# Kernel optimization log

Hardware: AMD Instinct MI355X
Metric: run time of the kernel (lower is better)

Reference implementation:

```python
import jax, jax.numpy as jnp
import numpy as np

D_MODEL = 1024
N_HEADS_Q = 16
N_HEADS_KV = 4
D_HEAD = 64  # d_qk = d_v
THETA = 10000.0
CLAMP = 80.0


def apply_rope(x, theta=THETA):
    # x: (b, h, s, d) with d even; interleaved-pair rotary embedding
    b, h, s, d = x.shape
    inv_freq = 1.0 / (theta ** (jnp.arange(0, d, 2, dtype=jnp.float32) / d))  # (d/2,)
    ang = jnp.arange(s, dtype=jnp.float32)[:, None] * inv_freq[None, :]       # (s, d/2)
    cos, sin = jnp.cos(ang), jnp.sin(ang)
    x1, x2 = x[..., 0::2], x[..., 1::2]
    o1 = x1 * cos - x2 * sin
    o2 = x1 * sin + x2 * cos
    return jnp.stack([o1, o2], axis=-1).reshape(b, h, s, d).astype(x.dtype)


def setup_inputs() -> dict:
    key = jax.random.key(0)
    k0, k1, k2, k3, k4 = jax.random.split(key, 5)
    scale = 1.0 / np.sqrt(D_MODEL)
    return {
        "x": jax.random.normal(k0, (2, 2048, D_MODEL), dtype=jnp.float32),
        "Wq": jax.random.normal(k1, (N_HEADS_Q * D_HEAD, D_MODEL), dtype=jnp.float32) * scale,
        "Wk": jax.random.normal(k2, (N_HEADS_KV * D_HEAD, D_MODEL), dtype=jnp.float32) * scale,
        "Wv": jax.random.normal(k3, (N_HEADS_KV * D_HEAD, D_MODEL), dtype=jnp.float32) * scale,
        "Wo": jax.random.normal(k4, (D_MODEL, N_HEADS_Q * D_HEAD), dtype=jnp.float32) * scale,
    }


def _attention(x, Wq, Wk, Wv, Wo):
    b, s, _ = x.shape
    r = N_HEADS_Q // N_HEADS_KV  # queries per KV group
    # projections (Linear: y = x @ W^T, no bias)
    Q = (x @ Wq.T).reshape(b, s, N_HEADS_Q, D_HEAD).transpose(0, 2, 1, 3)   # (b, Hq, s, d)
    K = (x @ Wk.T).reshape(b, s, N_HEADS_KV, D_HEAD).transpose(0, 2, 1, 3)  # (b, Hkv, s, d)
    V = (x @ Wv.T).reshape(b, s, N_HEADS_KV, D_HEAD).transpose(0, 2, 1, 3)
    Q = apply_rope(Q)
    K = apply_rope(K)
    # GQA grouping: (b, Hkv, r, s, d)
    Qg = Q.reshape(b, N_HEADS_KV, r, s, D_HEAD)
    scores = jnp.einsum('bgrqd,bgkd->bgrqk', Qg, K)          # (b, g, r, s, s)
    scores = jnp.clip(scores, -CLAMP, CLAMP)
    causal = jnp.tril(jnp.ones((s, s), dtype=bool))
    scores = jnp.where(causal, scores, -jnp.inf)
    weights = jax.nn.softmax(scores / jnp.sqrt(jnp.float32(D_HEAD)), axis=-1)
    attn = jnp.einsum('bgrqk,bgkd->bgrqd', weights, V)       # (b, g, r, s, d)
    # '... h_kv r s d -> ... s (h_kv r d)'
    attn = attn.transpose(0, 3, 1, 2, 4).reshape(b, s, N_HEADS_Q * D_HEAD)
    return attn @ Wo.T


def reference(x, Wq, Wk, Wv, Wo):
    return _attention(x, Wq, Wk, Wv, Wo)
```

## Files before the change

### kernel.cpp

```cpp
#include <hip/hip_runtime.h>
#include <hip/hip_bf16.h>
#include <math.h>

typedef __attribute__((ext_vector_type(8))) short bf16x8;
typedef __attribute__((ext_vector_type(4))) float f32x4;

#define B_   2
#define S_   2048
#define DM   1024
#define HQ   16
#define HKV  4
#define DH   64

#define MFMA16(a, b, c) __builtin_amdgcn_mfma_f32_16x16x32_bf16(a, b, c, 0, 0, 0)

__device__ __forceinline__ void load_lds16(const __hip_bfloat16* g, __hip_bfloat16* l)
{
    __builtin_amdgcn_global_load_lds(
        (const __attribute__((address_space(1))) unsigned int*)g,
        (__attribute__((address_space(3))) unsigned int*)l, 16, 0, 0);
}

#define CVT_TOTAL 6815744
__global__ void cvt_all(const float* __restrict__ x,  const float* __restrict__ wq,
                        const float* __restrict__ wk, const float* __restrict__ wv,
                        const float* __restrict__ wo,
                        __hip_bfloat16* __restrict__ xb,  __hip_bfloat16* __restrict__ wqb,
                        __hip_bfloat16* __restrict__ wkb, __hip_bfloat16* __restrict__ wvb,
                        __hip_bfloat16* __restrict__ wob)
{
    int i = (blockIdx.x * blockDim.x + threadIdx.x) * 4;
    if (i >= CVT_TOTAL) return;
    const float* src; __hip_bfloat16* dst; int off;
    if      (i < 4194304) { src = x;  dst = xb;  off = 0; }
    else if (i < 5242880) { src = wq; dst = wqb; off = 4194304; }
    else if (i < 5505024) { src = wk; dst = wkb; off = 5242880; }
    else if (i < 5767168) { src = wv; dst = wvb; off = 5505024; }
    else                  { src = wo; dst = wob; off = 5767168; }
    i -= off;
    float4 v = *(const float4*)(src + i);
    union { ushort4 u; __hip_bfloat16 h[4]; } p;
    p.h[0] = __float2bfloat16(v.x);
    p.h[1] = __float2bfloat16(v.y);
    p.h[2] = __float2bfloat16(v.z);
    p.h[3] = __float2bfloat16(v.w);
    *(ushort4*)(dst + i) = p.u;
}

template <bool QKV>
__global__ __launch_bounds__(256, 3) void gemm_tile(
    const __hip_bfloat16* __restrict__ A,
    const __hip_bfloat16* __restrict__ W,
    float* __restrict__ C0, __hip_bfloat16* __restrict__ Qb,
    __hip_bfloat16* __restrict__ Kb, __hip_bfloat16* __restrict__ Vt, int K)
{
    const int wave = threadIdx.x >> 6;
    const int lane = threadIdx.x & 63;
    const int quad = lane >> 4;
    const int l16  = lane & 15;
    const int wm = wave >> 1, wn = wave & 1;
    const int m0 = blockIdx.x * 64;
    const int n0 = blockIdx.y * 128;

    __shared__ __align__(16) __hip_bfloat16 As[64 * 32];
    __shared__ __align__(16) __hip_bfloat16 Bs[128 * 32];

    f32x4 acc[2][4] = {};

    for (int k0 = 0; k0 < K; k0 += 32) {
        #pragma unroll
        for (int r = 0; r < 3; ++r) {
            const int m = wave * 3 + r;
            if (m < 4) {
                const int g = m * 64 + lane;
                const int row = g >> 2;
                const int cbs = ((g & 3) - row) & 3;
                load_lds16(A + (size_t)(m0 + row) * K + k0 + cbs * 8, &As[m * 512]);
            } else {
                const int g = (m - 4) * 64 + lane;
                const int row = g >> 2;
                const int cbs = ((g & 3) - row) & 3;
                load_lds16(W + (size_t)(n0 + row) * K + k0 + cbs * 8, &Bs[(m - 4) * 512]);
            }
        }
        __syncthreads();
        bf16x8 af[2], bf[4];
        #pragma unroll
        for (int i = 0; i < 2; ++i) {
            const int ra = wm * 32 + i * 16 + l16;
            af[i] = *(const bf16x8*)&As[ra * 32 + ((quad + ra) & 3) * 8];
        }
        #pragma unroll
        for (int j = 0; j < 4; ++j) {
            const int rb = wn * 64 + j * 16 + l16;
            bf[j] = *(const bf16x8*)&Bs[rb * 32 + ((quad + rb) & 3) * 8];
        }
        #pragma unroll
        for (int i = 0; i < 2; ++i)
            #pragma unroll
            for (int j = 0; j < 4; ++j)
                acc[i][j] = MFMA16(af[i], bf[j], acc[i][j]);
        __syncthreads();
    }

    #pragma unroll
    for (int j = 0; j < 4; ++j) {
        const int cbase = n0 + wn * 64 + j * 16;
        const int cb = cbase + l16;
        if (QKV && cbase < 1280) {
            const int ii = (cb >> 1) & 31;
            const float f = exp2f((float)ii * -0.41524101186092f);
            const float f_rev = f * 0.15915494309189535f;
            const bool odd = cb & 1;
            #pragma unroll
            for (int i = 0; i < 2; ++i) {
                #pragma unroll
                for (int reg = 0; reg < 4; ++reg) {
                    const int row = m0 + wm * 32 + i * 16 + quad * 4 + reg;
                    const float v = acc[i][j][reg];
                    const float p = __shfl_xor(v, 1);
                    float rev = (float)(row & (S_ - 1)) * f_rev;
                    rev -= floorf(rev);
                    const float sn = __builtin_amdgcn_sinf(rev);
                    const float cs = __builtin_amdgcn_cosf(rev);
                    const float o = odd ? (p * sn + v * cs) : (v * cs - p * sn);
                    if (cbase < 1024)
                        Qb[(size_t)row * 1024 + cb] = __float2bfloat16(o);
                    else
                        Kb[(size_t)row * 256 + cb - 1024] = __float2bfloat16(o);
                }
            }
        } else {
            #pragma unroll
            for (int i = 0; i < 2; ++i) {
                #pragma unroll
                for (int reg = 0; reg < 4; ++reg) {
                    const int row = m0 + wm * 32 + i * 16 + quad * 4 + reg;
                    const float v = acc[i][j][reg];
                    if (QKV)
                        Vt[((size_t)(row >> 11) * 256 + (cb - 1280)) * S_ +
                           (row & (S_ - 1))] = __float2bfloat16(v);
                    else
                        C0[(size_t)row * 1024 + cb] = v;
                }
            }
        }
    }
}

template <bool MASKED>
__device__ __forceinline__ void softmax_store(
    const f32x4* sacc, int q, int k0, int quad, int l16,
    float& lsum, __hip_bfloat16* PsTile)
{
    #pragma unroll
    for (int nt = 0; nt < 4; ++nt) {
        union { ushort4 u; __hip_bfloat16 h[4]; } pk;
        #pragma unroll
        for (int reg = 0; reg < 4; ++reg) {
            const float sc = fminf(fmaxf(sacc[nt][reg], -80.0f), 80.0f);
            float p = exp2f(fmaf(sc, 0.18033688011112042f,
                                 -14.426950408889634f));
            if (MASKED) {
                const int key = k0 + nt * 16 + quad * 4 + reg;
                p = (key <= q) ? p : 0.0f;
            }
            lsum += p;
            pk.h[reg] = __float2bfloat16(p);
        }
        *(ushort4*)&PsTile[l16 * 72 + nt * 16 + quad * 4] = pk.u;
    }
}

__global__ __launch_bounds__(256, 2) void attn_mfma(
    const __hip_bfloat16* __restrict__ Q,
    const __hip_bfloat16* __restrict__ K,
    const __hip_bfloat16* __restrict__ Vt,
    __hip_bfloat16* __restrict__ ctx)
{
    const int t    = blockIdx.x & 15;
    const int hq   = (blockIdx.x >> 4) & (HQ - 1);
    const int b    = blockIdx.x >> 8;
    const int hkv  = hq >> 2;
    const int wave = threadIdx.x >> 6;
    const int lane = threadIdx.x & 63;
    const int quad = lane >> 4;
    const int l16  = lane & 15;

    const int qlo = t * 64 + wave * 16 + l16;
    const int qhi = (31 - t) * 64 + wave * 16 + l16;

    __shared__ __align__(16) __hip_bfloat16 Ks[2][64 * 64];
    __shared__ __align__(16) __hip_bfloat16 Vs[2][64 * 64];
    __shared__ __align__(16) __hip_bfloat16 Ps[4][2][16 * 72];

    const __hip_bfloat16* qpl = Q + ((size_t)(b * S_) + qlo) * (HQ * DH) + hq * DH + quad * 8;
    const __hip_bfloat16* qph = Q + ((size_t)(b * S_) + qhi) * (HQ * DH) + hq * DH + quad * 8;
    bf16x8 ql0 = *(const bf16x8*)qpl;
    bf16x8 ql1 = *(const bf16x8*)(qpl + 32);
    bf16x8 qh0 = *(const bf16x8*)qph;
    bf16x8 qh1 = *(const bf16x8*)(qph + 32);

    const __hip_bfloat16* Kg = K + (size_t)(b * S_) * (HKV * DH) + hkv * DH;
    const __hip_bfloat16* Vg = Vt + (size_t)(b * HKV + hkv) * DH * S_;

    auto stage = [&](int sb, int k0s) {
        #pragma unroll
        for (int r = 0; r < 2; ++r) {
            const int m = wave * 2 + r;
            const int g = m * 64 + lane;
            const int row = g >> 3;
            const int cbs = ((g & 7) - row) & 7;
            load_lds16(Kg + (size_t)(k0s + row) * (HKV * DH) + cbs * 8, &Ks[sb][m * 512]);
            load_lds16(Vg + (size_t)row * S_ + k0s + cbs * 8, &Vs[sb][m * 512]);
        }
    };

    stage(0, 0);

    float lsum_lo = 0.0f, lsum_hi = 0.0f;
    f32x4 Olo[4] = {}, Ohi[4] = {};
    const f32x4 zro = {0.0f, 0.0f, 0.0f, 0.0f};

    const int last = 31 - t;
    for (int kt = 0; kt <= last; ++kt) {
        const int buf = kt & 1;
        const int k0 = kt * 64;
        __syncthreads();
        if (kt < last) stage(buf ^ 1, k0 + 64);
        const bool dual = (kt <= t);

        bf16x8 ka[4][2];
        #pragma unroll
        for (int nt = 0; nt < 4; ++nt) {
            const int key = nt * 16 + l16;
            ka[nt][0] = *(const bf16x8*)&Ks[buf][key * 64 + ((quad + key) & 7) * 8];
            ka[nt][1] = *(const bf16x8*)&Ks[buf][key * 64 + ((quad + 4 + key) & 7) * 8];
        }
        f32x4 shi[4], slo[4];
        #pragma unroll
        for (int nt = 0; nt < 4; ++nt) {
            shi[nt] = MFMA16(ka[nt][0], qh0, zro);
            shi[nt] = MFMA16(ka[nt][1], qh1, shi[nt]);
        }
        if (dual) {
            #pragma unroll
            for (int nt = 0; nt < 4; ++nt) {
                slo[nt] = MFMA16(ka[nt][0], ql0, zro);
                slo[nt] = MFMA16(ka[nt][1], ql1, slo[nt]);
            }
        }

        if (kt == last) softmax_store<true >(shi, qhi, k0, quad, l16, lsum_hi, &Ps[wave][1][0]);
        else            softmax_store<false>(shi, qhi, k0, quad, l16, lsum_hi, &Ps[wave][1][0]);
        if (dual) {
            if (kt == t) softmax_store<true >(slo, qlo, k0, quad, l16, lsum_lo, &Ps[wave][0][0]);
            else         softmax_store<false>(slo, qlo, k0, quad, l16, lsum_lo, &Ps[wave][0][0]);
        }
        __asm__ __volatile__("s_waitcnt lgkmcnt(0)" ::: "memory");

        bf16x8 va[2][4];
        #pragma unroll
        for (int ks = 0; ks < 2; ++ks)
            #pragma unroll
            for (int dt = 0; dt < 4; ++dt) {
                const int d = dt * 16 + l16;
                va[ks][dt] = *(const bf16x8*)
                    &Vs[buf][d * 64 + ((ks * 4 + quad + d) & 7) * 8];
            }
        #pragma unroll
        for (int ks = 0; ks < 2; ++ks) {
            bf16x8 pb = *(const bf16x8*)&Ps[wave][1][l16 * 72 + ks * 32 + quad * 8];
            #pragma unroll
            for (int dt = 0; dt < 4; ++dt)
                Ohi[dt] = MFMA16(va[ks][dt], pb, Ohi[dt]);
        }
        if (dual) {
            #pragma unroll
            for (int ks = 0; ks < 2; ++ks) {
                bf16x8 pb = *(const bf16x8*)&Ps[wave][0][l16 * 72 + ks * 32 + quad * 8];
                #pragma unroll
                for (int dt = 0; dt < 4; ++dt)
                    Olo[dt] = MFMA16(va[ks][dt], pb, Olo[dt]);
            }
        }
    }

    auto finish = [&](float lsum, const f32x4* O, int qrow) {
        lsum += __shfl_xor(lsum, 16);
        lsum += __shfl_xor(lsum, 32);
        const float inv = 1.0f / lsum;
        __hip_bfloat16* cp =
            ctx + ((size_t)(b * S_) + qrow) * (HQ * DH) + hq * DH + quad * 4;
        #pragma unroll
        for (int dt = 0; dt < 4; ++dt) {
            union { ushort4 u; __hip_bfloat16 h[4]; } o;
            #pragma unroll
            for (int reg = 0; reg < 4; ++reg)
                o.h[reg] = __float2bfloat16(O[dt][reg] * inv);
            *(ushort4*)(cp + dt * 16) = o.u;
        }
    };
    finish(lsum_lo, Olo, qlo);
    finish(lsum_hi, Ohi, qhi);
}

extern "C" void kernel_launch(void* const* d_in, const int* in_sizes, int n_in,
                              void* d_out, int out_size, void* d_ws, size_t ws_size,
                              hipStream_t stream)
{
    const float* x  = (const float*)d_in[0];
    const float* Wq = (const float*)d_in[1];
    const float* Wk = (const float*)d_in[2];
    const float* Wv = (const float*)d_in[3];
    const float* Wo = (const float*)d_in[4];
    float* out = (float*)d_out;

    const int M = B_ * S_;

    char* w = (char*)d_ws;
    __hip_bfloat16* xb    = (__hip_bfloat16*)w;  w += (size_t)M * DM * 2;
    __hip_bfloat16* Wqkvb = (__hip_bfloat16*)w;  w += (size_t)1536 * DM * 2;
    __hip_bfloat16* Wob   = (__hip_bfloat16*)w;  w += (size_t)DM * (HQ * DH) * 2;
    __hip_bfloat16* Qb16  = (__hip_bfloat16*)w;  w += (size_t)M * (HQ * DH) * 2;
    __hip_bfloat16* Kb16  = (__hip_bfloat16*)w;  w += (size_t)M * (HKV * DH) * 2;
    __hip_bfloat16* Vt    = (__hip_bfloat16*)w;  w += (size_t)M * (HKV * DH) * 2;
    __hip_bfloat16* ctx   = (__hip_bfloat16*)w;

    __hip_bfloat16* Wqb = Wqkvb;
    __hip_bfloat16* Wkb = Wqkvb + (size_t)1024 * 1024;
    __hip_bfloat16* Wvb = Wqkvb + (size_t)1280 * 1024;

    cvt_all<<<(CVT_TOTAL / 4 + 255) / 256, 256, 0, stream>>>(
        x, Wq, Wk, Wv, Wo, xb, Wqb, Wkb, Wvb, Wob);

    gemm_tile<true><<<dim3(M / 64, 1536 / 128), 256, 0, stream>>>(
        xb, Wqkvb, nullptr, Qb16, Kb16, Vt, DM);

    attn_mfma<<<B_ * HQ * 16, 256, 0, stream>>>(Qb16, Kb16, Vt, ctx);

    gemm_tile<false><<<dim3(M / 64, 1024 / 128), 256, 0, stream>>>(
        ctx, Wob, out, nullptr, nullptr, nullptr, HQ * DH);
}
```

Before: 173.4 us.

## Load V fragments directly from global memory and swap PV MFMA operand order

V tiles are no longer staged through LDS. Each lane now loads its V^T fragments straight from global memory into registers at the start of each key tile, and the PV MFMA operands are swapped so P is the A operand. The output layout therefore changes: the finish step shuffles the per-row normalizer and writes scalar bf16 elements instead of ushort4 vectors. This removes the LDS traffic and footprint for V, which could help occupancy, but it adds uncached-latency global loads per iteration and less coalesced scalar stores.

```diff
diff --git a/kernel.cpp b/kernel.cpp
--- a/kernel.cpp
+++ b/kernel.cpp
@@ -187,11 +187,12 @@
     const int quad = lane >> 4;
     const int l16  = lane & 15;
 
-    const int qlo = t * 64 + wave * 16 + l16;
-    const int qhi = (31 - t) * 64 + wave * 16 + l16;
+    const int qb_lo = t * 64 + wave * 16;
+    const int qb_hi = (31 - t) * 64 + wave * 16;
+    const int qlo = qb_lo + l16;
+    const int qhi = qb_hi + l16;
 
     __shared__ __align__(16) __hip_bfloat16 Ks[2][64 * 64];
-    __shared__ __align__(16) __hip_bfloat16 Vs[2][64 * 64];
     __shared__ __align__(16) __hip_bfloat16 Ps[4][2][16 * 72];
 
     const __hip_bfloat16* qpl = Q + ((size_t)(b * S_) + qlo) * (HQ * DH) + hq * DH + quad * 8;
@@ -202,7 +203,8 @@
     bf16x8 qh1 = *(const bf16x8*)(qph + 32);
 
     const __hip_bfloat16* Kg = K + (size_t)(b * S_) * (HKV * DH) + hkv * DH;
-    const __hip_bfloat16* Vg = Vt + (size_t)(b * HKV + hkv) * DH * S_;
+    const __hip_bfloat16* Vb =
+        Vt + ((size_t)(b * HKV + hkv) * DH + l16) * S_ + quad * 8;
 
     auto stage = [&](int sb, int k0s) {
         #pragma unroll
@@ -212,7 +214,6 @@
             const int row = g >> 3;
             const int cbs = ((g & 7) - row) & 7;
             load_lds16(Kg + (size_t)(k0s + row) * (HKV * DH) + cbs * 8, &Ks[sb][m * 512]);
-            load_lds16(Vg + (size_t)row * S_ + k0s + cbs * 8, &Vs[sb][m * 512]);
         }
     };
 
@@ -230,6 +231,13 @@
         if (kt < last) stage(buf ^ 1, k0 + 64);
         const bool dual = (kt <= t);
 
+        bf16x8 vb[2][4];
+        #pragma unroll
+        for (int ks = 0; ks < 2; ++ks)
+            #pragma unroll
+            for (int dt = 0; dt < 4; ++dt)
+                vb[ks][dt] = *(const bf16x8*)(Vb + (size_t)dt * 16 * S_ + k0 + ks * 32);
+
         bf16x8 ka[4][2];
         #pragma unroll
         for (int nt = 0; nt < 4; ++nt) {
@@ -259,50 +267,40 @@
         }
         __asm__ __volatile__("s_waitcnt lgkmcnt(0)" ::: "memory");
 
-        bf16x8 va[2][4];
-        #pragma unroll
-        for (int ks = 0; ks < 2; ++ks)
-            #pragma unroll
-            for (int dt = 0; dt < 4; ++dt) {
-                const int d = dt * 16 + l16;
-                va[ks][dt] = *(const bf16x8*)
-                    &Vs[buf][d * 64 + ((ks * 4 + quad + d) & 7) * 8];
-            }
         #pragma unroll
         for (int ks = 0; ks < 2; ++ks) {
-            bf16x8 pb = *(const bf16x8*)&Ps[wave][1][l16 * 72 + ks * 32 + quad * 8];
+            bf16x8 pa = *(const bf16x8*)&Ps[wave][1][l16 * 72 + ks * 32 + quad * 8];
             #pragma unroll
             for (int dt = 0; dt < 4; ++dt)
-                Ohi[dt] = MFMA16(va[ks][dt], pb, Ohi[dt]);
+                Ohi[dt] = MFMA16(pa, vb[ks][dt], Ohi[dt]);
         }
         if (dual) {
             #pragma unroll
             for (int ks = 0; ks < 2; ++ks) {
-                bf16x8 pb = *(const bf16x8*)&Ps[wave][0][l16 * 72 + ks * 32 + quad * 8];
+                bf16x8 pa = *(const bf16x8*)&Ps[wave][0][l16 * 72 + ks * 32 + quad * 8];
                 #pragma unroll
                 for (int dt = 0; dt < 4; ++dt)
-                    Olo[dt] = MFMA16(va[ks][dt], pb, Olo[dt]);
+                    Olo[dt] = MFMA16(pa, vb[ks][dt], Olo[dt]);
             }
         }
     }
 
-    auto finish = [&](float lsum, const f32x4* O, int qrow) {
+    auto finish = [&](float lsum, const f32x4* O, int qbase) {
         lsum += __shfl_xor(lsum, 16);
         lsum += __shfl_xor(lsum, 32);
         const float inv = 1.0f / lsum;
-        __hip_bfloat16* cp =
-            ctx + ((size_t)(b * S_) + qrow) * (HQ * DH) + hq * DH + quad * 4;
-        #pragma unroll
-        for (int dt = 0; dt < 4; ++dt) {
-            union { ushort4 u; __hip_bfloat16 h[4]; } o;
-            #pragma unroll
-            for (int reg = 0; reg < 4; ++reg)
-                o.h[reg] = __float2bfloat16(O[dt][reg] * inv);
-            *(ushort4*)(cp + dt * 16) = o.u;
+        #pragma unroll
+        for (int reg = 0; reg < 4; ++reg) {
+            const float invr = __shfl(inv, quad * 4 + reg);
+            const int q = qbase + quad * 4 + reg;
+            __hip_bfloat16* cp = ctx + ((size_t)(b * S_) + q) * (HQ * DH) + hq * DH + l16;
+            #pragma unroll
+            for (int dt = 0; dt < 4; ++dt)
+                cp[dt * 16] = __float2bfloat16(O[dt][reg] * invr);
         }
     };
-    finish(lsum_lo, Olo, qlo);
-    finish(lsum_hi, Ohi, qhi);
+    finish(lsum_lo, Olo, qb_lo);
+    finish(lsum_hi, Ohi, qb_hi);
 }
 
 extern "C" void kernel_launch(void* const* d_in, const int* in_sizes, int n_in,
```

After: 200.4 us. +15.6%, slower.
